# Optimization experiments

Measured on AMD Instinct MI355X. Metric: run time of the kernel, lower is better.

## Reference

```python
import jax, jax.numpy as jnp
import numpy as np

C = 512          # resnet18 feature_dim
HID = 256        # relation_hidden_dim
B, Hh, Ww = 8, 14, 14


def setup_inputs() -> dict:
    key = jax.random.key(0)
    k1, k2, k3, k4, k5 = jax.random.split(key, 5)
    f1 = jax.random.normal(k1, (B, C, Hh, Ww), dtype=jnp.float32)
    f2 = jax.random.normal(k2, (B, C, Hh, Ww), dtype=jnp.float32)
    # relation head params (Linear(2C -> HID), ReLU, Linear(HID -> 1))
    s1 = 1.0 / np.sqrt(2 * C)
    s2 = 1.0 / np.sqrt(HID)
    W1 = jax.random.uniform(k3, (2 * C, HID), jnp.float32, -s1, s1)
    b1 = jnp.zeros((HID,), jnp.float32)
    W2 = jax.random.uniform(k4, (HID, 1), jnp.float32, -s2, s2)
    b2 = jnp.zeros((1,), jnp.float32)
    return {"f1": f1, "f2": f2, "W1": W1, "b1": b1, "W2": W2, "b2": b2}


def reference(f1, f2, W1, b1, W2, b2):
    # f1, f2: [B, C, h, w] encoder feature maps
    b, c, h, w = f1.shape
    L = h * w
    # [B, L, C]
    x1 = f1.reshape(b, c, L).transpose(0, 2, 1)
    x2 = f2.reshape(b, c, L).transpose(0, 2, 1)
    # Algebraic split of first Linear over the concat:
    # cat([f1_i, f2_j]) @ W1 == f1_i @ W1[:C] + f2_j @ W1[C:]
    p1 = jnp.einsum('blc,ch->blh', x1, W1[:c])      # [B, L, HID]
    p2 = jnp.einsum('blc,ch->blh', x2, W1[c:])      # [B, L, HID]
    hid = jax.nn.relu(p1[:, :, None, :] + p2[:, None, :, :] + b1)  # [B, L, L, HID]
    scores = jnp.einsum('bijh,ho->bijo', hid, W2) + b2  # [B, L, L, 1]
    sim = scores.reshape(b, L * L).sum(axis=1, keepdims=True)  # aggregation='sum'
    return sim
```

## Files before the change

### kernel.cpp

```cpp
#include <hip/hip_runtime.h>

typedef __attribute__((ext_vector_type(8))) short bf16x8;
typedef __attribute__((ext_vector_type(4))) float f32x4;

#define C_DIM 512
#define HID   256
#define B_DIM 8
#define L_DIM 196
#define MTPB  7
#define NT    32
#define NNT   (HID/NT)
#define GEMM_BLOCKS (B_DIM*MTPB*NNT*2)
#define ROWS  14
#define NJC   14
#define JCL   (L_DIM/NJC)
#define PAIR_BLOCKS ((B_DIM*NJC*ROWS)/4)
#define P_ELEMS (B_DIM*L_DIM*HID)

__device__ __forceinline__ short bf16r(float x) {
  unsigned u = __builtin_bit_cast(unsigned, x);
  return (short)((u + 0x8000u) >> 16);
}

__global__ __launch_bounds__(256) void gemm_p_mfma(
    const float* __restrict__ f1, const float* __restrict__ f2,
    const float* __restrict__ W1, const float* __restrict__ b1,
    const float* __restrict__ b2,
    float* __restrict__ p1, float* __restrict__ p2,
    float* __restrict__ out) {
  if (blockIdx.x == 0 && threadIdx.x < B_DIM)
    out[threadIdx.x] = (float)(L_DIM * L_DIM) * b2[0];

  const int wgid = blockIdx.x;
  const int b    = wgid & 7;
  const int idx  = wgid >> 3;
  const int nt   = idx & 7;
  const int ms   = idx >> 3;
  const int side = ms & 1;
  const int mt   = ms >> 1;

  const float* __restrict__ f = side ? f2 : f1;
  const float* __restrict__ W = W1 + side * C_DIM * HID;
  float* __restrict__ p = side ? p2 : p1;

  const int tid  = threadIdx.x;
  const int kq   = tid >> 6;
  const int lane = tid & 63;
  const int g    = lane >> 4;
  const int mcol = lane & 15;

  int aoff[2];
  #pragma unroll
  for (int mi = 0; mi < 2; ++mi) {
    const int rib = mt * 32 + mi * 16 + mcol;
    const int l = rib < L_DIM ? rib : L_DIM - 1;
    aoff[mi] = (b * C_DIM) * L_DIM + l;
  }
  const int h0 = nt * NT + mcol;

  f32x4 acc[2][2];
  #pragma unroll
  for (int mi = 0; mi < 2; ++mi)
    #pragma unroll
    for (int ni = 0; ni < 2; ++ni)
      acc[mi][ni] = (f32x4){0.f, 0.f, 0.f, 0.f};

  #pragma unroll
  for (int ks = 0; ks < 4; ++ks) {
    const int k0 = kq * 128 + ks * 32 + g * 8;
    bf16x8 afr[2], bfr[2];
    #pragma unroll
    for (int mi = 0; mi < 2; ++mi) {
      const float* __restrict__ pa = f + aoff[mi] + k0 * L_DIM;
      #pragma unroll
      for (int i = 0; i < 8; ++i) afr[mi][i] = bf16r(pa[i * L_DIM]);
    }
    #pragma unroll
    for (int ni = 0; ni < 2; ++ni) {
      const float* __restrict__ pb = W + k0 * HID + h0 + ni * 16;
      #pragma unroll
      for (int i = 0; i < 8; ++i) bfr[ni][i] = bf16r(pb[i * HID]);
    }
    #pragma unroll
    for (int mi = 0; mi < 2; ++mi)
      #pragma unroll
      for (int ni = 0; ni < 2; ++ni)
        acc[mi][ni] = __builtin_amdgcn_mfma_f32_16x16x32_bf16(
            afr[mi], bfr[ni], acc[mi][ni], 0, 0, 0);
  }

  __shared__ float comb[2][64][17];
  if (kq >= 2) {
    #pragma unroll
    for (int mi = 0; mi < 2; ++mi)
      #pragma unroll
      for (int ni = 0; ni < 2; ++ni)
        *(float4*)&comb[kq - 2][lane][mi * 8 + ni * 4] =
            *(float4*)&acc[mi][ni];
  }
  __syncthreads();
  if (kq < 2) {
    #pragma unroll
    for (int mi = 0; mi < 2; ++mi)
      #pragma unroll
      for (int ni = 0; ni < 2; ++ni) {
        const float4 o = *(const float4*)&comb[kq][lane][mi * 8 + ni * 4];
        acc[mi][ni][0] += o.x; acc[mi][ni][1] += o.y;
        acc[mi][ni][2] += o.z; acc[mi][ni][3] += o.w;
      }
  }
  __syncthreads();
  if (kq == 1) {
    #pragma unroll
    for (int mi = 0; mi < 2; ++mi)
      #pragma unroll
      for (int ni = 0; ni < 2; ++ni)
        *(float4*)&comb[0][lane][mi * 8 + ni * 4] = *(float4*)&acc[mi][ni];
  }
  __syncthreads();
  if (kq == 0) {
    #pragma unroll
    for (int mi = 0; mi < 2; ++mi) {
      const int rib0 = mt * 32 + mi * 16 + g * 4;
      #pragma unroll
      for (int ni = 0; ni < 2; ++ni) {
        const int h = h0 + ni * 16;
        const float bias = side ? 0.0f : b1[h];
        const float4 o = *(const float4*)&comb[0][lane][mi * 8 + ni * 4];
        const float v0 = acc[mi][ni][0] + o.x + bias;
        const float v1 = acc[mi][ni][1] + o.y + bias;
        const float v2 = acc[mi][ni][2] + o.z + bias;
        const float v3 = acc[mi][ni][3] + o.w + bias;
        if (rib0 + 0 < L_DIM) p[(b * L_DIM + rib0 + 0) * HID + h] = v0;
        if (rib0 + 1 < L_DIM) p[(b * L_DIM + rib0 + 1) * HID + h] = v1;
        if (rib0 + 2 < L_DIM) p[(b * L_DIM + rib0 + 2) * HID + h] = v2;
        if (rib0 + 3 < L_DIM) p[(b * L_DIM + rib0 + 3) * HID + h] = v3;
      }
    }
  }
}

__global__ __launch_bounds__(256) void pair_kernel(
    const float* __restrict__ p1, const float* __restrict__ p2,
    const float* __restrict__ W2, float* __restrict__ out) {
  const int lane = threadIdx.x & 63;
  const int w    = threadIdx.x >> 6;
  const int b    = blockIdx.x & 7;
  const int idx  = blockIdx.x >> 3;
  const int r4   = idx * 4 + w;
  const int jc   = r4 / ROWS;
  const int wi   = r4 % ROWS;

  const float4 wv = *(const float4*)(W2 + lane * 4);
  const float* __restrict__ p1b = p1 + (b * L_DIM) * HID + lane * 4;

  float4 a[ROWS];
  #pragma unroll
  for (int k = 0; k < ROWS; ++k)
    a[k] = *(const float4*)(p1b + (wi + k * ROWS) * HID);

  float s[ROWS];
  #pragma unroll
  for (int k = 0; k < ROWS; ++k) s[k] = 0.0f;

  const float4* __restrict__ vp =
      (const float4*)(p2 + (b * L_DIM + jc * JCL) * HID) + lane;

#define PAIR_BODY(vv)                                            \
  {                                                              \
    _Pragma("unroll")                                            \
    for (int k = 0; k < ROWS; ++k) {                             \
      s[k] = fmaf(fmaxf(a[k].x + (vv).x, 0.f), wv.x, s[k]);      \
      s[k] = fmaf(fmaxf(a[k].y + (vv).y, 0.f), wv.y, s[k]);      \
      s[k] = fmaf(fmaxf(a[k].z + (vv).z, 0.f), wv.z, s[k]);      \
      s[k] = fmaf(fmaxf(a[k].w + (vv).w, 0.f), wv.w, s[k]);      \
    }                                                            \
  }

  float4 vv[7];
  #pragma unroll
  for (int j = 0; j < 7; ++j) vv[j] = vp[j * (HID / 4)];
  #pragma unroll
  for (int j = 0; j < 7; ++j) PAIR_BODY(vv[j]);
  #pragma unroll
  for (int j = 0; j < 7; ++j) vv[j] = vp[(7 + j) * (HID / 4)];
  #pragma unroll
  for (int j = 0; j < 7; ++j) PAIR_BODY(vv[j]);
#undef PAIR_BODY

  float t = 0.0f;
  #pragma unroll
  for (int k = 0; k < ROWS; ++k) t += s[k];
  #pragma unroll
  for (int off = 32; off > 0; off >>= 1) t += __shfl_down(t, off);

  __shared__ float sred[4];
  if (lane == 0) sred[w] = t;
  __syncthreads();
  if (threadIdx.x == 0)
    atomicAdd(&out[b], sred[0] + sred[1] + sred[2] + sred[3]);
}

extern "C" void kernel_launch(void* const* d_in, const int* in_sizes, int n_in,
                              void* d_out, int out_size, void* d_ws, size_t ws_size,
                              hipStream_t stream) {
  const float* f1 = (const float*)d_in[0];
  const float* f2 = (const float*)d_in[1];
  const float* W1 = (const float*)d_in[2];
  const float* b1 = (const float*)d_in[3];
  const float* W2 = (const float*)d_in[4];
  const float* b2 = (const float*)d_in[5];
  float* out = (float*)d_out;

  float* p1 = (float*)d_ws;
  float* p2 = p1 + P_ELEMS;

  gemm_p_mfma<<<GEMM_BLOCKS, 256, 0, stream>>>(f1, f2, W1, b1, b2, p1, p2, out);

  pair_kernel<<<PAIR_BLOCKS, 256, 0, stream>>>(p1, p2, W2, out);
}
```

Measured before the change: 27.11 us.

## Pre-transpose features and weights to bf16 K-contiguous layout in a prep kernel

Adds a prep kernel that converts f1/f2 and W1 to bf16 and transposes them so the reduction dimension is contiguous. The GEMM then loads each MFMA fragment with a single 16-byte vector load instead of eight strided scalar fp32 loads plus conversions. This is meant to cut uncoalesced, strided global traffic in the GEMM. In exchange it adds a third kernel launch and an extra round trip through workspace memory for the transposed copies, which matters at this small problem size.

```diff
diff --git a/kernel.cpp b/kernel.cpp
--- a/kernel.cpp
+++ b/kernel.cpp
@@ -9,23 +9,57 @@
 #define L_DIM 196
 #define MTPB  7
 #define NT    32
-#define NNT   (HID/NT)
-#define GEMM_BLOCKS (B_DIM*MTPB*NNT*2)
+#define GEMM_BLOCKS (B_DIM*MTPB*8*2)
 #define ROWS  14
 #define NJC   14
 #define JCL   (L_DIM/NJC)
 #define PAIR_BLOCKS ((B_DIM*NJC*ROWS)/4)
 #define P_ELEMS (B_DIM*L_DIM*HID)
+#define FT_ROWS (2*B_DIM*L_DIM)
+#define WT_ROWS (2*HID)
 
 __device__ __forceinline__ short bf16r(float x) {
   unsigned u = __builtin_bit_cast(unsigned, x);
   return (short)((u + 0x8000u) >> 16);
 }
 
+__global__ __launch_bounds__(256) void prep_kernel(
+    const float* __restrict__ f1, const float* __restrict__ f2,
+    const float* __restrict__ W1,
+    unsigned short* __restrict__ fT, unsigned short* __restrict__ WT) {
+  const int w    = threadIdx.x >> 6;
+  const int lane = threadIdx.x & 63;
+  const int bid  = blockIdx.x;
+  if (bid < 1024) {
+    const int b    = bid & 7;
+    const int idx  = bid >> 3;
+    const int side = idx >> 6;
+    const int co   = idx & 63;
+    const int l0   = (w < 3) ? w * 64 : 132;
+    const int l    = l0 + lane;
+    const float* __restrict__ f = side ? f2 : f1;
+    const float* __restrict__ src = f + (b * C_DIM + co * 8) * L_DIM + l;
+    bf16x8 v;
+    #pragma unroll
+    for (int i = 0; i < 8; ++i) v[i] = bf16r(src[i * L_DIM]);
+    *(bf16x8*)(fT + ((size_t)(side * (B_DIM * L_DIM) + b * L_DIM + l) << 9)
+                  + co * 8) = v;
+  } else {
+    const int wid  = bid - 1024;
+    const int side = wid >> 6;
+    const int co   = wid & 63;
+    const int h    = w * 64 + lane;
+    const float* __restrict__ src = W1 + (side * C_DIM + co * 8) * HID + h;
+    bf16x8 v;
+    #pragma unroll
+    for (int i = 0; i < 8; ++i) v[i] = bf16r(src[i * HID]);
+    *(bf16x8*)(WT + ((size_t)(side * HID + h) << 9) + co * 8) = v;
+  }
+}
+
 __global__ __launch_bounds__(256) void gemm_p_mfma(
-    const float* __restrict__ f1, const float* __restrict__ f2,
-    const float* __restrict__ W1, const float* __restrict__ b1,
-    const float* __restrict__ b2,
+    const unsigned short* __restrict__ fT, const unsigned short* __restrict__ WT,
+    const float* __restrict__ b1, const float* __restrict__ b2,
     float* __restrict__ p1, float* __restrict__ p2,
     float* __restrict__ out) {
   if (blockIdx.x == 0 && threadIdx.x < B_DIM)
@@ -39,8 +73,6 @@
   const int side = ms & 1;
   const int mt   = ms >> 1;
 
-  const float* __restrict__ f = side ? f2 : f1;
-  const float* __restrict__ W = W1 + side * C_DIM * HID;
   float* __restrict__ p = side ? p2 : p1;
 
   const int tid  = threadIdx.x;
@@ -49,12 +81,12 @@
   const int g    = lane >> 4;
   const int mcol = lane & 15;
 
-  int aoff[2];
+  int rowA[2];
   #pragma unroll
   for (int mi = 0; mi < 2; ++mi) {
     const int rib = mt * 32 + mi * 16 + mcol;
     const int l = rib < L_DIM ? rib : L_DIM - 1;
-    aoff[mi] = (b * C_DIM) * L_DIM + l;
+    rowA[mi] = side * (B_DIM * L_DIM) + b * L_DIM + l;
   }
   const int h0 = nt * NT + mcol;
 
@@ -70,17 +102,11 @@
     const int k0 = kq * 128 + ks * 32 + g * 8;
     bf16x8 afr[2], bfr[2];
     #pragma unroll
-    for (int mi = 0; mi < 2; ++mi) {
-      const float* __restrict__ pa = f + aoff[mi] + k0 * L_DIM;
-      #pragma unroll
-      for (int i = 0; i < 8; ++i) afr[mi][i] = bf16r(pa[i * L_DIM]);
-    }
-    #pragma unroll
-    for (int ni = 0; ni < 2; ++ni) {
-      const float* __restrict__ pb = W + k0 * HID + h0 + ni * 16;
-      #pragma unroll
-      for (int i = 0; i < 8; ++i) bfr[ni][i] = bf16r(pb[i * HID]);
-    }
+    for (int mi = 0; mi < 2; ++mi)
+      afr[mi] = *(const bf16x8*)(fT + ((size_t)rowA[mi] << 9) + k0);
+    #pragma unroll
+    for (int ni = 0; ni < 2; ++ni)
+      bfr[ni] = *(const bf16x8*)(WT + ((size_t)(side * HID + h0 + ni * 16) << 9) + k0);
     #pragma unroll
     for (int mi = 0; mi < 2; ++mi)
       #pragma unroll
@@ -214,8 +240,12 @@
 
   float* p1 = (float*)d_ws;
   float* p2 = p1 + P_ELEMS;
-
-  gemm_p_mfma<<<GEMM_BLOCKS, 256, 0, stream>>>(f1, f2, W1, b1, b2, p1, p2, out);
+  unsigned short* fT = (unsigned short*)(p2 + P_ELEMS);
+  unsigned short* WT = fT + (size_t)FT_ROWS * 512;
+
+  prep_kernel<<<1152, 256, 0, stream>>>(f1, f2, W1, fT, WT);
+
+  gemm_p_mfma<<<GEMM_BLOCKS, 256, 0, stream>>>(fT, WT, b1, b2, p1, p2, out);
 
   pair_kernel<<<PAIR_BLOCKS, 256, 0, stream>>>(p1, p2, W2, out);
 }
```

Result: slower. 31.37 us (+15.7%).
